# Optimization experiments

Hardware: AMD Instinct MI355X
Metric: run time of the kernel (lower is better)

## Reference

```python
import jax, jax.numpy as jnp
import numpy as np

B, S, H = 16, 64, 4096
NH, NKV, HD = 32, 8, 128
G = NH // NKV
L_CACHE = 4608
ROPE_THETA = 1e6


def setup_inputs() -> dict:
    key = jax.random.key(0)
    ks = jax.random.split(key, 12)
    hidden_states = jax.random.normal(ks[0], (B, S, H), jnp.float32)
    k_cache = jax.random.normal(ks[1], (B, L_CACHE, NKV, HD), jnp.float32)
    v_cache = jax.random.normal(ks[2], (B, L_CACHE, NKV, HD), jnp.float32)
    wq = jax.random.normal(ks[3], (H, H), jnp.float32) * 0.02
    bq = jax.random.normal(ks[4], (H,), jnp.float32) * 0.02
    wk = jax.random.normal(ks[5], (NKV * HD, H), jnp.float32) * 0.02
    bk = jax.random.normal(ks[6], (NKV * HD,), jnp.float32) * 0.02
    wv = jax.random.normal(ks[7], (NKV * HD, H), jnp.float32) * 0.02
    bv = jax.random.normal(ks[8], (NKV * HD,), jnp.float32) * 0.02
    wo = jax.random.normal(ks[9], (H, H), jnp.float32) * 0.02
    cache_lens = jax.random.randint(ks[10], (B,), 2048, 4096, jnp.int32)
    # RoPE cos/sin at absolute positions cache_lens + [0..S)
    inv_freq = 1.0 / (ROPE_THETA ** (jnp.arange(0, HD, 2, dtype=jnp.float32) / HD))
    pos = (cache_lens[:, None] + jnp.arange(S)[None, :]).astype(jnp.float32)  # (B,S)
    freqs = pos[..., None] * inv_freq  # (B,S,HD/2)
    emb = jnp.concatenate([freqs, freqs], axis=-1)  # (B,S,HD)
    cos, sin = jnp.cos(emb), jnp.sin(emb)
    # tree mask: lower-triangular (chain) tree, diagonal included so every query attends
    tree_mask = jnp.tril(jnp.ones((S, S), jnp.bool_))[None].repeat(B, axis=0)
    return {"hidden_states": hidden_states, "cos": cos, "sin": sin,
            "k_cache": k_cache, "v_cache": v_cache,
            "wq": wq, "bq": bq, "wk": wk, "bk": bk, "wv": wv, "bv": bv, "wo": wo,
            "cache_lens": cache_lens, "tree_mask": tree_mask}


def reference(hidden_states, cos, sin, k_cache, v_cache, wq, bq, wk, bk, wv, bv, wo,
              cache_lens, tree_mask):
    scale = 1.0 / jnp.sqrt(jnp.float32(HD))

    def rope(x):  # x: (B,S,h,HD); cos/sin broadcast on head dim (unsqueeze_dim=2)
        x1, x2 = jnp.split(x, 2, axis=-1)
        rot = jnp.concatenate([-x2, x1], axis=-1)
        return x * cos[:, :, None, :] + rot * sin[:, :, None, :]

    q = (hidden_states @ wq.T + bq).reshape(B, S, NH, HD)
    k = (hidden_states @ wk.T + bk).reshape(B, S, NKV, HD)
    v = (hidden_states @ wv.T + bv).reshape(B, S, NKV, HD)
    q, k = rope(q), rope(k)

    # group q heads per kv head: head h = n*G + g (matches repeat_interleave ordering)
    qg = q.reshape(B, S, NKV, G, HD)

    # --- prefix attention against KV cache (flash_attn_with_kvcache semantics) ---
    L = k_cache.shape[1]
    ps = jnp.einsum('bsngd,blnd->bngsl', qg, k_cache) * scale  # (B,NKV,G,S,L)
    valid = jnp.arange(L)[None, :] < cache_lens[:, None]  # (B,L)
    ps = jnp.where(valid[:, None, None, None, :], ps, -jnp.inf)
    prefix_lse = jax.nn.logsumexp(ps, axis=-1)  # (B,NKV,G,S)
    prefix_o = jnp.einsum('bngsl,blnd->bsngd', jax.nn.softmax(ps, axis=-1), v_cache)

    # --- append current k/v into cache and gather (current_kv_len == all_kv_len == S) ---
    pos = cache_lens[:, None] + jnp.arange(S)[None, :]  # (B,S)
    bidx = jnp.arange(B)[:, None]
    k_cache = k_cache.at[bidx, pos].set(k)
    v_cache = v_cache.at[bidx, pos].set(v)
    kc = k_cache[bidx, pos]  # (B,S,NKV,HD)
    vc = v_cache[bidx, pos]

    # --- tree-masked attention over the speculative block ---
    cs = jnp.einsum('bsngd,btnd->bngst', qg, kc) * scale  # (B,NKV,G,S,S)
    cs = jnp.where(tree_mask[:, None, None, :, :], cs, -jnp.inf)
    cur_lse = jax.nn.logsumexp(cs, axis=-1)  # (B,NKV,G,S)
    cur_o = jnp.einsum('bngst,btnd->bsngd', jax.nn.softmax(cs, axis=-1), vc)

    # --- LSE merge of prefix and tree branches ---
    plse = prefix_lse.transpose(0, 3, 1, 2).reshape(B, S, NH)[..., None]
    clse = cur_lse.transpose(0, 3, 1, 2).reshape(B, S, NH)[..., None]
    w = jax.nn.sigmoid(plse - clse)  # (B,S,NH,1)
    out = prefix_o.reshape(B, S, NH, HD) * w + cur_o.reshape(B, S, NH, HD) * (1.0 - w)
    return out.reshape(B, S, H) @ wo.T
```

## Files before the change

### kernel.cpp

```cpp
#include <hip/hip_runtime.h>
#include <stdint.h>
#include <stddef.h>

#define Bb 16
#define Ss 64
#define Hh 4096
#define NKVv 8
#define HDd 128
#define LCACHE 4608
#define MM (Bb*Ss)
#define NQKV (Hh + 2*NKVv*HDd)
#define SCALE_Q 0.08838834764831845f
#define SPLITS 8

typedef float fx4 __attribute__((ext_vector_type(4)));
typedef short s16x8 __attribute__((ext_vector_type(8)));
typedef unsigned short u16;
typedef unsigned short u16x8 __attribute__((ext_vector_type(8)));
typedef unsigned short u16x4 __attribute__((ext_vector_type(4)));

__device__ __forceinline__ u16 f2bf(float f) {
  union { float f; unsigned u; } x; x.f = f;
  unsigned r = x.u + 0x7FFFu + ((x.u >> 16) & 1u);
  return (u16)(r >> 16);
}

__device__ __forceinline__ float bf2f(u16 v) {
  union { unsigned u; float f; } x; x.u = ((unsigned)v) << 16; return x.f;
}

__device__ __forceinline__ fx4 MFMA(s16x8 a, s16x8 b, fx4 c) {
  return __builtin_amdgcn_mfma_f32_16x16x32_bf16(a, b, c, 0, 0, 0);
}

__device__ __forceinline__ void gl_lds16(const void* g, void* l) {
  __builtin_amdgcn_global_load_lds(
      (const __attribute__((address_space(1))) void*)g,
      (__attribute__((address_space(3))) void*)l, 16, 0, 0);
}

__global__ __launch_bounds__(256) void cast_bf16_kernel(
    const float* __restrict__ src, u16* __restrict__ dst, int n8) {
  int i = blockIdx.x * 256 + threadIdx.x;
  if (i >= n8) return;
  fx4 a = *(const fx4*)(src + (size_t)i * 8);
  fx4 b = *(const fx4*)(src + (size_t)i * 8 + 4);
  u16x8 o;
  o[0]=f2bf(a[0]); o[1]=f2bf(a[1]); o[2]=f2bf(a[2]); o[3]=f2bf(a[3]);
  o[4]=f2bf(b[0]); o[5]=f2bf(b[1]); o[6]=f2bf(b[2]); o[7]=f2bf(b[3]);
  *(u16x8*)(dst + (size_t)i * 8) = o;
}

__global__ __launch_bounds__(256) void addf_kernel(
    const float* __restrict__ a, const float* __restrict__ b,
    float* __restrict__ out, int n8) {
  int i = blockIdx.x * 256 + threadIdx.x;
  if (i >= n8) return;
  fx4 x0 = *(const fx4*)(a + (size_t)i * 8);
  fx4 x1 = *(const fx4*)(a + (size_t)i * 8 + 4);
  fx4 y0 = *(const fx4*)(b + (size_t)i * 8);
  fx4 y1 = *(const fx4*)(b + (size_t)i * 8 + 4);
  *(fx4*)(out + (size_t)i * 8)     = x0 + y0;
  *(fx4*)(out + (size_t)i * 8 + 4) = x1 + y1;
}

__global__ __launch_bounds__(256) void gemm_bt_kernel(
    const u16* __restrict__ A, const u16* __restrict__ W,
    const float* __restrict__ bias, float* __restrict__ C,
    int M, int N, int K)
{
  __shared__ __align__(16) u16 As[128*32];
  __shared__ __align__(16) u16 Ws[128*32];
  const int t = threadIdx.x;
  const int lane = t & 63, w = t >> 6;
  const int wr = (w >> 1) * 64, wc = (w & 1) * 64;
  const int lr = lane & 15, lg = lane >> 4;
  const int mt = blockIdx.y * 128, nt = blockIdx.x * 128;
  const int kz = K >> 1;
  const int kbeg = blockIdx.z * kz, kend = kbeg + kz;
  C += (size_t)blockIdx.z * M * N;

  fx4 acc[4][4];
#pragma unroll
  for (int i = 0; i < 4; i++)
#pragma unroll
    for (int j = 0; j < 4; j++) acc[i][j] = (fx4){0.f,0.f,0.f,0.f};

  const int r = t >> 2;
  const int cg = (t & 3) ^ (r & 3);
  const u16* Ag0 = A + (size_t)(mt + r) * K + cg*8;
  const u16* Ag1 = A + (size_t)(mt + 64 + r) * K + cg*8;
  const u16* Wg0 = W + (size_t)(nt + r) * K + cg*8;
  const u16* Wg1 = W + (size_t)(nt + 64 + r) * K + cg*8;
  const int wvb = (t >> 6) * 1024;

  for (int k0 = kbeg; k0 < kend; k0 += 32) {
    __syncthreads();
    gl_lds16(Ag0 + k0, (char*)As + wvb);
    gl_lds16(Ag1 + k0, (char*)As + 4096 + wvb);
    gl_lds16(Wg0 + k0, (char*)Ws + wvb);
    gl_lds16(Wg1 + k0, (char*)Ws + 4096 + wvb);
    __syncthreads();
    s16x8 af[4], bfr[4];
    const int csw = (lg ^ (lr & 3)) * 8;
#pragma unroll
    for (int i = 0; i < 4; i++)
      af[i] = *(const s16x8*)(As + (wr + i*16 + lr)*32 + csw);
#pragma unroll
    for (int j = 0; j < 4; j++)
      bfr[j] = *(const s16x8*)(Ws + (wc + j*16 + lr)*32 + csw);
#pragma unroll
    for (int i = 0; i < 4; i++)
#pragma unroll
      for (int j = 0; j < 4; j++)
        acc[i][j] = MFMA(af[i], bfr[j], acc[i][j]);
  }

#pragma unroll
  for (int j = 0; j < 4; j++) {
    const int col = nt + wc + j*16 + lr;
    const float bv = (bias && blockIdx.z == 0) ? bias[col] : 0.0f;
#pragma unroll
    for (int i = 0; i < 4; i++) {
      const int row0 = mt + wr + i*16 + lg*4;
#pragma unroll
      for (int q = 0; q < 4; q++)
        C[(size_t)(row0 + q) * N + col] = acc[i][j][q] + bv;
    }
  }
}

__global__ __launch_bounds__(256) void rope_split_kernel(
    const float* __restrict__ qkv, const float* __restrict__ cosb,
    const float* __restrict__ sinb, u16* __restrict__ qb,
    u16* __restrict__ kb, u16* __restrict__ vb)
{
  const int wt = blockIdx.x * 4 + (threadIdx.x >> 6);
  const int lane = threadIdx.x & 63;
  const int m = wt / 48;
  const int task = wt - m * 48;
  const int b = m >> 6, s = m & 63;
  const float* row0 = qkv + (size_t)m * NQKV;
  const float* row1 = row0 + (size_t)MM * NQKV;

  if (task < 32) {
    const int h = task;
    const float x1 = row0[h*128 + lane]      + row1[h*128 + lane];
    const float x2 = row0[h*128 + 64 + lane] + row1[h*128 + 64 + lane];
    const float c = cosb[m*128 + lane];
    const float sn = sinb[m*128 + lane];
    u16* dst = qb + (((size_t)(b*8 + (h>>2)))*256 + (h&3)*64 + s) * 128;
    dst[lane]      = f2bf((x1*c - x2*sn) * SCALE_Q);
    dst[lane + 64] = f2bf((x2*c + x1*sn) * SCALE_Q);
  } else if (task < 40) {
    const int n = task - 32;
    const float x1 = row0[4096 + n*128 + lane]      + row1[4096 + n*128 + lane];
    const float x2 = row0[4096 + n*128 + 64 + lane] + row1[4096 + n*128 + 64 + lane];
    const float c = cosb[m*128 + lane];
    const float sn = sinb[m*128 + lane];
    u16* dst = kb + (((size_t)(b*8 + n))*64 + s) * 128;
    dst[lane]      = f2bf(x1*c - x2*sn);
    dst[lane + 64] = f2bf(x2*c + x1*sn);
  } else {
    const int n = task - 40;
    const float x1 = row0[5120 + n*128 + lane]      + row1[5120 + n*128 + lane];
    const float x2 = row0[5120 + n*128 + 64 + lane] + row1[5120 + n*128 + 64 + lane];
    u16* dst = vb + (((size_t)(b*8 + n))*64 + s) * 128;
    dst[lane]      = f2bf(x1);
    dst[lane + 64] = f2bf(x2);
  }
}

__global__ __launch_bounds__(512) void flash_kernel(
    const u16* __restrict__ qb, const u16* __restrict__ kb, const u16* __restrict__ vb,
    const float* __restrict__ kc, const float* __restrict__ vc,
    const int* __restrict__ cache_lens,
    u16* __restrict__ Op, float* __restrict__ lv)
{
  __shared__ __align__(16) u16 Kt[64*128];
  __shared__ __align__(16) u16 Vt[128*64];
  __shared__ __align__(16) u16 Pl[8*32*64];

  const int wid = blockIdx.x;
  const int split = wid & (SPLITS-1);
  const int bn = wid >> 3;
  const int b = bn >> 3, n = bn & 7;
  const int t = threadIdx.x;
  const int lane = t & 63, w = t >> 6;
  const int lr = lane & 15, lg = lane >> 4;
  const int L = cache_lens[b];

  s16x8 qf[2][4];
  const u16* qbase = qb + ((size_t)bn*256 + w*32) * 128;
#pragma unroll
  for (int rf = 0; rf < 2; rf++)
#pragma unroll
    for (int ks = 0; ks < 4; ks++)
      qf[rf][ks] = *(const s16x8*)(qbase + (rf*16 + lr)*128 + ks*32 + lg*8);

  fx4 O[2][8];
  float l_r[2];
#pragma unroll
  for (int rf = 0; rf < 2; rf++) {
    l_r[rf] = 0.f;
#pragma unroll
    for (int cn = 0; cn < 8; cn++) O[rf][cn] = (fx4){0.f,0.f,0.f,0.f};
  }

  const int ntile = (L + 63) >> 6;
  const int chunk = (ntile + SPLITS - 1) / SPLITS;
  const int t0 = split * chunk;
  int t1 = min(t0 + chunk, ntile); if (t1 < t0) t1 = t0;
  const bool last = (split == SPLITS - 1);
  const int tend = last ? t1 + 1 : t1;

  const int krow = t >> 3, kcol = (t & 7) * 16;
  const int vd0 = (t >> 4) * 4, vr0 = (t & 15) * 4;
  char* pw = (char*)Pl + w * 4096;

  const float* kbase = kc + (((size_t)b*LCACHE + krow)*NKVv + n)*HDd + kcol;
  const float* vbase = vc + (((size_t)b*LCACHE + vr0)*NKVv + n)*HDd + vd0;

  fx4 kr0, kr1, kr2, kr3;
#define ISSUEK(tile_) do { \
    const float* ks_ = kbase + (size_t)(tile_) * (64*NKVv*HDd); \
    kr0 = *(const fx4*)(ks_);     kr1 = *(const fx4*)(ks_ + 4); \
    kr2 = *(const fx4*)(ks_ + 8); kr3 = *(const fx4*)(ks_ + 12); \
  } while (0)

  if (t0 < t1) ISSUEK(t0);

  for (int tile = t0; tile < tend; ++tile) {
    const bool cur = (tile == t1);
    const int l0 = tile * 64;
    __syncthreads();
    if (!cur) {
      const float* srcv = vbase + (size_t)tile * (64*NKVv*HDd);
      fx4 vv0 = *(const fx4*)(srcv);
      fx4 vv1 = *(const fx4*)(srcv + NKVv*HDd);
      fx4 vv2 = *(const fx4*)(srcv + 2*NKVv*HDd);
      fx4 vv3 = *(const fx4*)(srcv + 3*NKVv*HDd);
      {
        u16x8 v8;
        v8[0]=f2bf(kr0[0]); v8[1]=f2bf(kr0[1]); v8[2]=f2bf(kr0[2]); v8[3]=f2bf(kr0[3]);
        v8[4]=f2bf(kr1[0]); v8[5]=f2bf(kr1[1]); v8[6]=f2bf(kr1[2]); v8[7]=f2bf(kr1[3]);
        int byt = (krow*256 + kcol*2) ^ ((krow & 7) << 4);
        *(u16x8*)((char*)Kt + byt) = v8;
        v8[0]=f2bf(kr2[0]); v8[1]=f2bf(kr2[1]); v8[2]=f2bf(kr2[2]); v8[3]=f2bf(kr2[3]);
        v8[4]=f2bf(kr3[0]); v8[5]=f2bf(kr3[1]); v8[6]=f2bf(kr3[2]); v8[7]=f2bf(kr3[3]);
        byt = (krow*256 + (kcol + 8)*2) ^ ((krow & 7) << 4);
        *(u16x8*)((char*)Kt + byt) = v8;
      }
      if (tile + 1 < t1) ISSUEK(tile + 1);
      {
#pragma unroll
        for (int dd = 0; dd < 4; dd++) {
          u16x4 pk;
          pk[0]=f2bf(vv0[dd]); pk[1]=f2bf(vv1[dd]); pk[2]=f2bf(vv2[dd]); pk[3]=f2bf(vv3[dd]);
          const int d = vd0 + dd;
          const int byt = (d*128 + vr0*2) ^ ((d & 7) << 4);
          *(u16x4*)((char*)Vt + byt) = pk;
        }
      }
    } else {
      {
        const u16* src = kb + ((size_t)bn*64 + krow)*128 + kcol;
        u16x8 a0 = *(const u16x8*)(src);
        u16x8 a1 = *(const u16x8*)(src + 8);
        int byt = (krow*256 + kcol*2) ^ ((krow & 7) << 4);
        *(u16x8*)((char*)Kt + byt) = a0;
        byt = (krow*256 + (kcol + 8)*2) ^ ((krow & 7) << 4);
        *(u16x8*)((char*)Kt + byt) = a1;
      }
      {
        const u16* srcv = vb + (size_t)bn*8192 + (size_t)vr0*128 + vd0;
        u16x4 tv0 = *(const u16x4*)(srcv);
        u16x4 tv1 = *(const u16x4*)(srcv + 128);
        u16x4 tv2 = *(const u16x4*)(srcv + 256);
        u16x4 tv3 = *(const u16x4*)(srcv + 384);
#pragma unroll
        for (int dd = 0; dd < 4; dd++) {
          u16x4 pk; pk[0]=tv0[dd]; pk[1]=tv1[dd]; pk[2]=tv2[dd]; pk[3]=tv3[dd];
          const int d = vd0 + dd;
          const int byt = (d*128 + vr0*2) ^ ((d & 7) << 4);
          *(u16x4*)((char*)Vt + byt) = pk;
        }
      }
    }
    __syncthreads();

#pragma unroll
    for (int cf = 0; cf < 4; cf++) {
      s16x8 kf[4];
      const int trow = cf*16 + lr;
#pragma unroll
      for (int ks = 0; ks < 4; ks++) {
        const int byt = (trow*256 + (ks*32 + lg*8)*2) ^ ((trow & 7) << 4);
        kf[ks] = *(const s16x8*)((char*)Kt + byt);
      }
#pragma unroll
      for (int rf = 0; rf < 2; rf++) {
        fx4 s = {0.f,0.f,0.f,0.f};
#pragma unroll
        for (int ks = 0; ks < 4; ks++) s = MFMA(kf[ks], qf[rf][ks], s);
        if (cur) {
          const int s0 = ((w*32 + rf*16) & 48) + lr;
#pragma unroll
          for (int i = 0; i < 4; i++)
            if (cf*16 + lg*4 + i > s0) s[i] = -1e30f;
        } else if (l0 + 64 > L) {
          const int kvp = l0 + cf*16 + lg*4;
#pragma unroll
          for (int i = 0; i < 4; i++)
            if (kvp + i >= L) s[i] = -1e30f;
        }
        u16x4 pk;
#pragma unroll
        for (int i = 0; i < 4; i++) {
          const float e = __expf(s[i]);
          l_r[rf] += e;
          pk[i] = f2bf(e);
        }
        const int row = rf*16 + lr;
        const int byt = (row*128 + (cf*16 + lg*4)*2) ^ ((row & 7) << 4);
        *(u16x4*)(pw + byt) = pk;
      }
    }

#pragma unroll
    for (int ksv = 0; ksv < 2; ksv++) {
#pragma unroll
      for (int rf = 0; rf < 2; rf++) {
        const int row = rf*16 + lr;
        const int byt = (row*128 + (ksv*32 + lg*8)*2) ^ ((row & 7) << 4);
        const s16x8 pf = *(const s16x8*)(pw + byt);
#pragma unroll
        for (int cn = 0; cn < 8; cn++) {
          const int c = cn*16 + lr;
          const int bytv = (c*128 + (ksv*32 + lg*8)*2) ^ ((c & 7) << 4);
          const s16x8 vf = *(const s16x8*)((char*)Vt + bytv);
          O[rf][cn] = MFMA(pf, vf, O[rf][cn]);
        }
      }
    }
  }

  const size_t pbase = ((size_t)bn*SPLITS + split) * 256;
#pragma unroll
  for (int rf = 0; rf < 2; rf++) {
    float lt = l_r[rf];
    lt += __shfl_xor(lt, 16);
    lt += __shfl_xor(lt, 32);
    if (lg == 0) lv[pbase + w*32 + rf*16 + lr] = lt;
#pragma unroll
    for (int i = 0; i < 4; i++) {
      const int prow = w*32 + rf*16 + lg*4 + i;
      u16* dst = Op + (pbase + prow)*128;
#pragma unroll
      for (int cn = 0; cn < 8; cn++)
        dst[cn*16 + lr] = f2bf(O[rf][cn][i]);
    }
  }
}

__global__ __launch_bounds__(256) void merge_kernel(
    const u16* __restrict__ Op, const float* __restrict__ lv,
    u16* __restrict__ attn)
{
  const int gid = blockIdx.x * 4 + (threadIdx.x >> 6);
  const int lane = threadIdx.x & 63;
  const int bn = gid >> 8, prow = gid & 255;
  const int b = bn >> 3, n = bn & 7;
  const int g = prow >> 6, srow = prow & 63;

  float ltot = 0.f;
#pragma unroll
  for (int s = 0; s < SPLITS; s++)
    ltot += lv[((size_t)bn*SPLITS + s)*256 + prow];
  const float inv = 1.f / ltot;

  float ox = 0.f, oy = 0.f;
#pragma unroll
  for (int s = 0; s < SPLITS; s++) {
    const u16* src = Op + (((size_t)bn*SPLITS + s)*256 + prow)*128 + lane*2;
    ox += bf2f(src[0]);
    oy += bf2f(src[1]);
  }
  u16* dst = attn + ((size_t)(b*64 + srow))*4096 + (size_t)(n*4 + g)*128 + lane*2;
  dst[0] = f2bf(ox * inv);
  dst[1] = f2bf(oy * inv);
}

extern "C" void kernel_launch(void* const* d_in, const int* in_sizes, int n_in,
                              void* d_out, int out_size, void* d_ws, size_t ws_size,
                              hipStream_t stream) {
  (void)in_sizes; (void)n_in; (void)out_size; (void)ws_size;
  const float* hidden = (const float*)d_in[0];
  const float* cosb   = (const float*)d_in[1];
  const float* sinb   = (const float*)d_in[2];
  const float* kc     = (const float*)d_in[3];
  const float* vc     = (const float*)d_in[4];
  const float* wq     = (const float*)d_in[5];
  const float* bq     = (const float*)d_in[6];
  const float* wk     = (const float*)d_in[7];
  const float* bk     = (const float*)d_in[8];
  const float* wv     = (const float*)d_in[9];
  const float* bv     = (const float*)d_in[10];
  const float* wo     = (const float*)d_in[11];
  const int* clens    = (const int*)d_in[12];
  float* out = (float*)d_out;

  char* ws = (char*)d_ws;
  size_t off = 0;
  auto alloc = [&](size_t bytes) -> void* {
    void* p = ws + off; off += (bytes + 255) & ~(size_t)255; return p;
  };
  u16* Wqkv  = (u16*)alloc((size_t)NQKV * Hh * 2);
  u16* Xb    = (u16*)alloc((size_t)MM * Hh * 2);
  float* qkvf= (float*)alloc((size_t)2 * MM * NQKV * 4);
  u16* qbuf  = (u16*)alloc((size_t)Bb*NKVv*256*HDd*2);
  u16* kbuf  = (u16*)alloc((size_t)Bb*NKVv*64*HDd*2);
  u16* vbuf  = (u16*)alloc((size_t)Bb*NKVv*64*HDd*2);
  float* biasq = (float*)alloc((size_t)NQKV * 4);
  u16* Op    = (u16*)alloc((size_t)Bb*NKVv*SPLITS*256*128*2);
  float* lv  = (float*)alloc((size_t)Bb*NKVv*SPLITS*256*4);

  hipMemcpyAsync(biasq,        bq, 4096*sizeof(float), hipMemcpyDeviceToDevice, stream);
  hipMemcpyAsync(biasq + 4096, bk, 1024*sizeof(float), hipMemcpyDeviceToDevice, stream);
  hipMemcpyAsync(biasq + 5120, bv, 1024*sizeof(float), hipMemcpyDeviceToDevice, stream);

  auto cast = [&](const float* s, u16* d, size_t nelem) {
    int n8 = (int)(nelem / 8);
    cast_bf16_kernel<<<(n8 + 255) / 256, 256, 0, stream>>>(s, d, n8);
  };
  cast(hidden, Xb, (size_t)MM * Hh);
  cast(wq, Wqkv,                      (size_t)4096 * 4096);
  cast(wk, Wqkv + (size_t)4096*4096,  (size_t)1024 * 4096);
  cast(wv, Wqkv + (size_t)5120*4096,  (size_t)1024 * 4096);

  gemm_bt_kernel<<<dim3(NQKV/128, MM/128, 2), 256, 0, stream>>>(Xb, Wqkv, biasq, qkvf, MM, NQKV, Hh);
  rope_split_kernel<<<(MM*48)/4, 256, 0, stream>>>(qkvf, cosb, sinb, qbuf, kbuf, vbuf);

  u16* Wo = Wqkv;
  cast(wo, Wo, (size_t)4096 * 4096);

  flash_kernel<<<Bb*NKVv*SPLITS, 512, 0, stream>>>(qbuf, kbuf, vbuf, kc, vc, clens, Op, lv);

  u16* attn = Xb;
  merge_kernel<<<(Bb*NKVv*256)/4, 256, 0, stream>>>(Op, lv, attn);

  float* Cp = qkvf;
  gemm_bt_kernel<<<dim3(Hh/128, MM/128, 2), 256, 0, stream>>>(attn, Wo, nullptr, Cp, MM, Hh, Hh);
  addf_kernel<<<((MM*Hh/8) + 255)/256, 256, 0, stream>>>(Cp, Cp + (size_t)MM*Hh, out, MM*Hh/8);
}
```

Measured before the change: 377.8 us.

## Drop split-K GEMMs, use 128x64 tiles with XCD remap, fuse casts, add MFMA priority

Replaces the split-K=2 GEMMs, which wrote two fp32 partials that were then summed, with single-pass GEMMs on 128x64 tiles and an XCD-aware block remap. This removes the extra partial-sum traffic, the addf kernel and the doubled reads in rope. All five fp32-to-bf16 casts are merged into one launch, with Wo getting its own buffer. The flash kernel wraps its MFMA sections in s_setprio and reuses each V fragment for both row tiles. Each GEMM now runs fewer, longer blocks (768 and 512), which may reduce latency hiding compared with split-K.

```diff
diff --git a/kernel.cpp b/kernel.cpp
--- a/kernel.cpp
+++ b/kernel.cpp
@@ -39,29 +39,26 @@
       (__attribute__((address_space(3))) void*)l, 16, 0, 0);
 }
 
-__global__ __launch_bounds__(256) void cast_bf16_kernel(
-    const float* __restrict__ src, u16* __restrict__ dst, int n8) {
-  int i = blockIdx.x * 256 + threadIdx.x;
-  if (i >= n8) return;
-  fx4 a = *(const fx4*)(src + (size_t)i * 8);
-  fx4 b = *(const fx4*)(src + (size_t)i * 8 + 4);
+__global__ __launch_bounds__(256) void cast_all_kernel(
+    const float* __restrict__ hid, const float* __restrict__ wq,
+    const float* __restrict__ wk, const float* __restrict__ wv,
+    const float* __restrict__ wo, u16* __restrict__ xb,
+    u16* __restrict__ wqkv, u16* __restrict__ wob)
+{
+  const int bid = blockIdx.x;
+  const float* src; u16* dst; long i;
+  if (bid < 2048)       { src = hid; dst = xb;   i = (long)bid * 256; }
+  else if (bid < 10240) { src = wq;  dst = wqkv; i = (long)(bid - 2048) * 256; }
+  else if (bid < 12288) { src = wk;  dst = wqkv + (size_t)4096*4096; i = (long)(bid - 10240) * 256; }
+  else if (bid < 14336) { src = wv;  dst = wqkv + (size_t)5120*4096; i = (long)(bid - 12288) * 256; }
+  else                  { src = wo;  dst = wob;  i = (long)(bid - 14336) * 256; }
+  i += threadIdx.x;
+  fx4 a = *(const fx4*)(src + i * 8);
+  fx4 b = *(const fx4*)(src + i * 8 + 4);
   u16x8 o;
   o[0]=f2bf(a[0]); o[1]=f2bf(a[1]); o[2]=f2bf(a[2]); o[3]=f2bf(a[3]);
   o[4]=f2bf(b[0]); o[5]=f2bf(b[1]); o[6]=f2bf(b[2]); o[7]=f2bf(b[3]);
-  *(u16x8*)(dst + (size_t)i * 8) = o;
-}
-
-__global__ __launch_bounds__(256) void addf_kernel(
-    const float* __restrict__ a, const float* __restrict__ b,
-    float* __restrict__ out, int n8) {
-  int i = blockIdx.x * 256 + threadIdx.x;
-  if (i >= n8) return;
-  fx4 x0 = *(const fx4*)(a + (size_t)i * 8);
-  fx4 x1 = *(const fx4*)(a + (size_t)i * 8 + 4);
-  fx4 y0 = *(const fx4*)(b + (size_t)i * 8);
-  fx4 y1 = *(const fx4*)(b + (size_t)i * 8 + 4);
-  *(fx4*)(out + (size_t)i * 8)     = x0 + y0;
-  *(fx4*)(out + (size_t)i * 8 + 4) = x1 + y1;
+  *(u16x8*)(dst + i * 8) = o;
 }
 
 __global__ __launch_bounds__(256) void gemm_bt_kernel(
@@ -70,56 +67,59 @@
     int M, int N, int K)
 {
   __shared__ __align__(16) u16 As[128*32];
-  __shared__ __align__(16) u16 Ws[128*32];
+  __shared__ __align__(16) u16 Ws[64*32];
   const int t = threadIdx.x;
   const int lane = t & 63, w = t >> 6;
-  const int wr = (w >> 1) * 64, wc = (w & 1) * 64;
+  const int wr = (w >> 1) * 64, wc = (w & 1) * 32;
   const int lr = lane & 15, lg = lane >> 4;
-  const int mt = blockIdx.y * 128, nt = blockIdx.x * 128;
-  const int kz = K >> 1;
-  const int kbeg = blockIdx.z * kz, kend = kbeg + kz;
-  C += (size_t)blockIdx.z * M * N;
-
-  fx4 acc[4][4];
+
+  const int nwg = gridDim.x;
+  const int cpx = nwg >> 3;
+  const int wid = (blockIdx.x & 7) * cpx + (blockIdx.x >> 3);
+  const int Nt = N >> 6;
+  const int nt = (wid % Nt) * 64;
+  const int mt = (wid / Nt) * 128;
+
+  fx4 acc[4][2];
 #pragma unroll
   for (int i = 0; i < 4; i++)
 #pragma unroll
-    for (int j = 0; j < 4; j++) acc[i][j] = (fx4){0.f,0.f,0.f,0.f};
+    for (int j = 0; j < 2; j++) acc[i][j] = (fx4){0.f,0.f,0.f,0.f};
 
   const int r = t >> 2;
   const int cg = (t & 3) ^ (r & 3);
   const u16* Ag0 = A + (size_t)(mt + r) * K + cg*8;
   const u16* Ag1 = A + (size_t)(mt + 64 + r) * K + cg*8;
   const u16* Wg0 = W + (size_t)(nt + r) * K + cg*8;
-  const u16* Wg1 = W + (size_t)(nt + 64 + r) * K + cg*8;
-  const int wvb = (t >> 6) * 1024;
-
-  for (int k0 = kbeg; k0 < kend; k0 += 32) {
+  const int wvb = w * 1024;
+
+  for (int k0 = 0; k0 < K; k0 += 32) {
     __syncthreads();
     gl_lds16(Ag0 + k0, (char*)As + wvb);
     gl_lds16(Ag1 + k0, (char*)As + 4096 + wvb);
     gl_lds16(Wg0 + k0, (char*)Ws + wvb);
-    gl_lds16(Wg1 + k0, (char*)Ws + 4096 + wvb);
     __syncthreads();
-    s16x8 af[4], bfr[4];
+    s16x8 af[4], bfr[2];
     const int csw = (lg ^ (lr & 3)) * 8;
 #pragma unroll
     for (int i = 0; i < 4; i++)
       af[i] = *(const s16x8*)(As + (wr + i*16 + lr)*32 + csw);
 #pragma unroll
-    for (int j = 0; j < 4; j++)
+    for (int j = 0; j < 2; j++)
       bfr[j] = *(const s16x8*)(Ws + (wc + j*16 + lr)*32 + csw);
+    __builtin_amdgcn_s_setprio(1);
 #pragma unroll
     for (int i = 0; i < 4; i++)
 #pragma unroll
-      for (int j = 0; j < 4; j++)
+      for (int j = 0; j < 2; j++)
         acc[i][j] = MFMA(af[i], bfr[j], acc[i][j]);
-  }
-
-#pragma unroll
-  for (int j = 0; j < 4; j++) {
+    __builtin_amdgcn_s_setprio(0);
+  }
+
+#pragma unroll
+  for (int j = 0; j < 2; j++) {
     const int col = nt + wc + j*16 + lr;
-    const float bv = (bias && blockIdx.z == 0) ? bias[col] : 0.0f;
+    const float bv = bias ? bias[col] : 0.0f;
 #pragma unroll
     for (int i = 0; i < 4; i++) {
       const int row0 = mt + wr + i*16 + lg*4;
@@ -140,13 +140,12 @@
   const int m = wt / 48;
   const int task = wt - m * 48;
   const int b = m >> 6, s = m & 63;
-  const float* row0 = qkv + (size_t)m * NQKV;
-  const float* row1 = row0 + (size_t)MM * NQKV;
+  const float* row = qkv + (size_t)m * NQKV;
 
   if (task < 32) {
     const int h = task;
-    const float x1 = row0[h*128 + lane]      + row1[h*128 + lane];
-    const float x2 = row0[h*128 + 64 + lane] + row1[h*128 + 64 + lane];
+    const float x1 = row[h*128 + lane];
+    const float x2 = row[h*128 + 64 + lane];
     const float c = cosb[m*128 + lane];
     const float sn = sinb[m*128 + lane];
     u16* dst = qb + (((size_t)(b*8 + (h>>2)))*256 + (h&3)*64 + s) * 128;
@@ -154,8 +153,8 @@
     dst[lane + 64] = f2bf((x2*c + x1*sn) * SCALE_Q);
   } else if (task < 40) {
     const int n = task - 32;
-    const float x1 = row0[4096 + n*128 + lane]      + row1[4096 + n*128 + lane];
-    const float x2 = row0[4096 + n*128 + 64 + lane] + row1[4096 + n*128 + 64 + lane];
+    const float x1 = row[4096 + n*128 + lane];
+    const float x2 = row[4096 + n*128 + 64 + lane];
     const float c = cosb[m*128 + lane];
     const float sn = sinb[m*128 + lane];
     u16* dst = kb + (((size_t)(b*8 + n))*64 + s) * 128;
@@ -163,8 +162,8 @@
     dst[lane + 64] = f2bf(x2*c + x1*sn);
   } else {
     const int n = task - 40;
-    const float x1 = row0[5120 + n*128 + lane]      + row1[5120 + n*128 + lane];
-    const float x2 = row0[5120 + n*128 + 64 + lane] + row1[5120 + n*128 + 64 + lane];
+    const float x1 = row[5120 + n*128 + lane];
+    const float x2 = row[5120 + n*128 + 64 + lane];
     u16* dst = vb + (((size_t)(b*8 + n))*64 + s) * 128;
     dst[lane]      = f2bf(x1);
     dst[lane + 64] = f2bf(x2);
@@ -298,11 +297,19 @@
         const int byt = (trow*256 + (ks*32 + lg*8)*2) ^ ((trow & 7) << 4);
         kf[ks] = *(const s16x8*)((char*)Kt + byt);
       }
+      fx4 sc2[2];
+      __builtin_amdgcn_s_setprio(1);
 #pragma unroll
       for (int rf = 0; rf < 2; rf++) {
         fx4 s = {0.f,0.f,0.f,0.f};
 #pragma unroll
         for (int ks = 0; ks < 4; ks++) s = MFMA(kf[ks], qf[rf][ks], s);
+        sc2[rf] = s;
+      }
+      __builtin_amdgcn_s_setprio(0);
+#pragma unroll
+      for (int rf = 0; rf < 2; rf++) {
+        fx4 s = sc2[rf];
         if (cur) {
           const int s0 = ((w*32 + rf*16) & 48) + lr;
 #pragma unroll
@@ -329,19 +336,20 @@
 
 #pragma unroll
     for (int ksv = 0; ksv < 2; ksv++) {
-#pragma unroll
-      for (int rf = 0; rf < 2; rf++) {
-        const int row = rf*16 + lr;
-        const int byt = (row*128 + (ksv*32 + lg*8)*2) ^ ((row & 7) << 4);
-        const s16x8 pf = *(const s16x8*)(pw + byt);
-#pragma unroll
-        for (int cn = 0; cn < 8; cn++) {
-          const int c = cn*16 + lr;
-          const int bytv = (c*128 + (ksv*32 + lg*8)*2) ^ ((c & 7) << 4);
-          const s16x8 vf = *(const s16x8*)((char*)Vt + bytv);
-          O[rf][cn] = MFMA(pf, vf, O[rf][cn]);
-        }
-      }
+      const int bytp0 = (lr*128 + (ksv*32 + lg*8)*2) ^ ((lr & 7) << 4);
+      const s16x8 pf0 = *(const s16x8*)(pw + bytp0);
+      const int bytp1 = ((16 + lr)*128 + (ksv*32 + lg*8)*2) ^ ((lr & 7) << 4);
+      const s16x8 pf1 = *(const s16x8*)(pw + bytp1);
+      __builtin_amdgcn_s_setprio(1);
+#pragma unroll
+      for (int cn = 0; cn < 8; cn++) {
+        const int c = cn*16 + lr;
+        const int bytv = (c*128 + (ksv*32 + lg*8)*2) ^ ((c & 7) << 4);
+        const s16x8 vf = *(const s16x8*)((char*)Vt + bytv);
+        O[0][cn] = MFMA(pf0, vf, O[0][cn]);
+        O[1][cn] = MFMA(pf1, vf, O[1][cn]);
+      }
+      __builtin_amdgcn_s_setprio(0);
     }
   }
 
@@ -416,8 +424,9 @@
     void* p = ws + off; off += (bytes + 255) & ~(size_t)255; return p;
   };
   u16* Wqkv  = (u16*)alloc((size_t)NQKV * Hh * 2);
+  u16* Wob   = (u16*)alloc((size_t)Hh * Hh * 2);
   u16* Xb    = (u16*)alloc((size_t)MM * Hh * 2);
-  float* qkvf= (float*)alloc((size_t)2 * MM * NQKV * 4);
+  float* qkvf= (float*)alloc((size_t)MM * NQKV * 4);
   u16* qbuf  = (u16*)alloc((size_t)Bb*NKVv*256*HDd*2);
   u16* kbuf  = (u16*)alloc((size_t)Bb*NKVv*64*HDd*2);
   u16* vbuf  = (u16*)alloc((size_t)Bb*NKVv*64*HDd*2);
@@ -429,27 +438,15 @@
   hipMemcpyAsync(biasq + 4096, bk, 1024*sizeof(float), hipMemcpyDeviceToDevice, stream);
   hipMemcpyAsync(biasq + 5120, bv, 1024*sizeof(float), hipMemcpyDeviceToDevice, stream);
 
-  auto cast = [&](const float* s, u16* d, size_t nelem) {
-    int n8 = (int)(nelem / 8);
-    cast_bf16_kernel<<<(n8 + 255) / 256, 256, 0, stream>>>(s, d, n8);
-  };
-  cast(hidden, Xb, (size_t)MM * Hh);
-  cast(wq, Wqkv,                      (size_t)4096 * 4096);
-  cast(wk, Wqkv + (size_t)4096*4096,  (size_t)1024 * 4096);
-  cast(wv, Wqkv + (size_t)5120*4096,  (size_t)1024 * 4096);
-
-  gemm_bt_kernel<<<dim3(NQKV/128, MM/128, 2), 256, 0, stream>>>(Xb, Wqkv, biasq, qkvf, MM, NQKV, Hh);
+  cast_all_kernel<<<22528, 256, 0, stream>>>(hidden, wq, wk, wv, wo, Xb, Wqkv, Wob);
+
+  gemm_bt_kernel<<<768, 256, 0, stream>>>(Xb, Wqkv, biasq, qkvf, MM, NQKV, Hh);
   rope_split_kernel<<<(MM*48)/4, 256, 0, stream>>>(qkvf, cosb, sinb, qbuf, kbuf, vbuf);
-
-  u16* Wo = Wqkv;
-  cast(wo, Wo, (size_t)4096 * 4096);
 
   flash_kernel<<<Bb*NKVv*SPLITS, 512, 0, stream>>>(qbuf, kbuf, vbuf, kc, vc, clens, Op, lv);
 
   u16* attn = Xb;
   merge_kernel<<<(Bb*NKVv*256)/4, 256, 0, stream>>>(Op, lv, attn);
 
-  float* Cp = qkvf;
-  gemm_bt_kernel<<<dim3(Hh/128, MM/128, 2), 256, 0, stream>>>(attn, Wo, nullptr, Cp, MM, Hh, Hh);
-  addf_kernel<<<((MM*Hh/8) + 255)/256, 256, 0, stream>>>(Cp, Cp + (size_t)MM*Hh, out, MM*Hh/8);
-}
+  gemm_bt_kernel<<<512, 256, 0, stream>>>(attn, Wob, nullptr, out, MM, Hh, Hh);
+}
```

Result: slower. 403.3 us (+6.7%).

## Fuse input casts, drop bias memcpys, add MFMA setprio and share V fragments

Applied to the files above, without the earlier changes.

Replaces the four separate fp32-to-bf16 cast launches with one combined cast kernel. It also removes the three device-to-device bias copies by having the GEMM epilogue pick bq, bk or bv by column. The GEMM and flash kernels wrap their MFMA bursts in s_setprio to favour matrix issue. The PV loop now loads each V fragment once and reuses it for both row fragments, which cuts LDS reads. Together these reduce launch and copy overhead, at the cost of a per-column branch in the epilogue.

```diff
diff --git a/kernel.cpp b/kernel.cpp
--- a/kernel.cpp
+++ b/kernel.cpp
@@ -37,6 +37,26 @@
   __builtin_amdgcn_global_load_lds(
       (const __attribute__((address_space(1))) void*)g,
       (__attribute__((address_space(3))) void*)l, 16, 0, 0);
+}
+
+__global__ __launch_bounds__(256) void cast_all_kernel(
+    const float* __restrict__ hid, const float* __restrict__ wq,
+    const float* __restrict__ wk, const float* __restrict__ wv,
+    u16* __restrict__ xb, u16* __restrict__ wqkv)
+{
+  const int bid = blockIdx.x;
+  const float* src; u16* dst; long i;
+  if (bid < 2048)       { src = hid; dst = xb;   i = (long)bid * 256; }
+  else if (bid < 10240) { src = wq;  dst = wqkv; i = (long)(bid - 2048) * 256; }
+  else if (bid < 12288) { src = wk;  dst = wqkv + (size_t)4096*4096; i = (long)(bid - 10240) * 256; }
+  else                  { src = wv;  dst = wqkv + (size_t)5120*4096; i = (long)(bid - 12288) * 256; }
+  i += threadIdx.x;
+  fx4 a = *(const fx4*)(src + i * 8);
+  fx4 b = *(const fx4*)(src + i * 8 + 4);
+  u16x8 o;
+  o[0]=f2bf(a[0]); o[1]=f2bf(a[1]); o[2]=f2bf(a[2]); o[3]=f2bf(a[3]);
+  o[4]=f2bf(b[0]); o[5]=f2bf(b[1]); o[6]=f2bf(b[2]); o[7]=f2bf(b[3]);
+  *(u16x8*)(dst + i * 8) = o;
 }
 
 __global__ __launch_bounds__(256) void cast_bf16_kernel(
@@ -66,7 +86,8 @@
 
 __global__ __launch_bounds__(256) void gemm_bt_kernel(
     const u16* __restrict__ A, const u16* __restrict__ W,
-    const float* __restrict__ bias, float* __restrict__ C,
+    const float* __restrict__ bqp, const float* __restrict__ bkp,
+    const float* __restrict__ bvp, float* __restrict__ C,
     int M, int N, int K)
 {
   __shared__ __align__(16) u16 As[128*32];
@@ -92,7 +113,7 @@
   const u16* Ag1 = A + (size_t)(mt + 64 + r) * K + cg*8;
   const u16* Wg0 = W + (size_t)(nt + r) * K + cg*8;
   const u16* Wg1 = W + (size_t)(nt + 64 + r) * K + cg*8;
-  const int wvb = (t >> 6) * 1024;
+  const int wvb = w * 1024;
 
   for (int k0 = kbeg; k0 < kend; k0 += 32) {
     __syncthreads();
@@ -109,23 +130,27 @@
 #pragma unroll
     for (int j = 0; j < 4; j++)
       bfr[j] = *(const s16x8*)(Ws + (wc + j*16 + lr)*32 + csw);
+    __builtin_amdgcn_s_setprio(1);
 #pragma unroll
     for (int i = 0; i < 4; i++)
 #pragma unroll
       for (int j = 0; j < 4; j++)
         acc[i][j] = MFMA(af[i], bfr[j], acc[i][j]);
+    __builtin_amdgcn_s_setprio(0);
   }
 
 #pragma unroll
   for (int j = 0; j < 4; j++) {
     const int col = nt + wc + j*16 + lr;
-    const float bv = (bias && blockIdx.z == 0) ? bias[col] : 0.0f;
+    float bv_ = 0.0f;
+    if (bqp && blockIdx.z == 0)
+      bv_ = col < 4096 ? bqp[col] : (col < 5120 ? bkp[col - 4096] : bvp[col - 5120]);
 #pragma unroll
     for (int i = 0; i < 4; i++) {
       const int row0 = mt + wr + i*16 + lg*4;
 #pragma unroll
       for (int q = 0; q < 4; q++)
-        C[(size_t)(row0 + q) * N + col] = acc[i][j][q] + bv;
+        C[(size_t)(row0 + q) * N + col] = acc[i][j][q] + bv_;
     }
   }
 }
@@ -298,11 +323,19 @@
         const int byt = (trow*256 + (ks*32 + lg*8)*2) ^ ((trow & 7) << 4);
         kf[ks] = *(const s16x8*)((char*)Kt + byt);
       }
+      fx4 sc2[2];
+      __builtin_amdgcn_s_setprio(1);
 #pragma unroll
       for (int rf = 0; rf < 2; rf++) {
         fx4 s = {0.f,0.f,0.f,0.f};
 #pragma unroll
         for (int ks = 0; ks < 4; ks++) s = MFMA(kf[ks], qf[rf][ks], s);
+        sc2[rf] = s;
+      }
+      __builtin_amdgcn_s_setprio(0);
+#pragma unroll
+      for (int rf = 0; rf < 2; rf++) {
+        fx4 s = sc2[rf];
         if (cur) {
           const int s0 = ((w*32 + rf*16) & 48) + lr;
 #pragma unroll
@@ -329,19 +362,20 @@
 
 #pragma unroll
     for (int ksv = 0; ksv < 2; ksv++) {
-#pragma unroll
-      for (int rf = 0; rf < 2; rf++) {
-        const int row = rf*16 + lr;
-        const int byt = (row*128 + (ksv*32 + lg*8)*2) ^ ((row & 7) << 4);
-        const s16x8 pf = *(const s16x8*)(pw + byt);
-#pragma unroll
-        for (int cn = 0; cn < 8; cn++) {
-          const int c = cn*16 + lr;
-          const int bytv = (c*128 + (ksv*32 + lg*8)*2) ^ ((c & 7) << 4);
-          const s16x8 vf = *(const s16x8*)((char*)Vt + bytv);
-          O[rf][cn] = MFMA(pf, vf, O[rf][cn]);
-        }
-      }
+      const int bytp0 = (lr*128 + (ksv*32 + lg*8)*2) ^ ((lr & 7) << 4);
+      const s16x8 pf0 = *(const s16x8*)(pw + bytp0);
+      const int bytp1 = ((16 + lr)*128 + (ksv*32 + lg*8)*2) ^ ((lr & 7) << 4);
+      const s16x8 pf1 = *(const s16x8*)(pw + bytp1);
+      __builtin_amdgcn_s_setprio(1);
+#pragma unroll
+      for (int cn = 0; cn < 8; cn++) {
+        const int c = cn*16 + lr;
+        const int bytv = (c*128 + (ksv*32 + lg*8)*2) ^ ((c & 7) << 4);
+        const s16x8 vf = *(const s16x8*)((char*)Vt + bytv);
+        O[0][cn] = MFMA(pf0, vf, O[0][cn]);
+        O[1][cn] = MFMA(pf1, vf, O[1][cn]);
+      }
+      __builtin_amdgcn_s_setprio(0);
     }
   }
 
@@ -421,28 +455,17 @@
   u16* qbuf  = (u16*)alloc((size_t)Bb*NKVv*256*HDd*2);
   u16* kbuf  = (u16*)alloc((size_t)Bb*NKVv*64*HDd*2);
   u16* vbuf  = (u16*)alloc((size_t)Bb*NKVv*64*HDd*2);
-  float* biasq = (float*)alloc((size_t)NQKV * 4);
   u16* Op    = (u16*)alloc((size_t)Bb*NKVv*SPLITS*256*128*2);
   float* lv  = (float*)alloc((size_t)Bb*NKVv*SPLITS*256*4);
 
-  hipMemcpyAsync(biasq,        bq, 4096*sizeof(float), hipMemcpyDeviceToDevice, stream);
-  hipMemcpyAsync(biasq + 4096, bk, 1024*sizeof(float), hipMemcpyDeviceToDevice, stream);
-  hipMemcpyAsync(biasq + 5120, bv, 1024*sizeof(float), hipMemcpyDeviceToDevice, stream);
-
-  auto cast = [&](const float* s, u16* d, size_t nelem) {
-    int n8 = (int)(nelem / 8);
-    cast_bf16_kernel<<<(n8 + 255) / 256, 256, 0, stream>>>(s, d, n8);
-  };
-  cast(hidden, Xb, (size_t)MM * Hh);
-  cast(wq, Wqkv,                      (size_t)4096 * 4096);
-  cast(wk, Wqkv + (size_t)4096*4096,  (size_t)1024 * 4096);
-  cast(wv, Wqkv + (size_t)5120*4096,  (size_t)1024 * 4096);
-
-  gemm_bt_kernel<<<dim3(NQKV/128, MM/128, 2), 256, 0, stream>>>(Xb, Wqkv, biasq, qkvf, MM, NQKV, Hh);
+  cast_all_kernel<<<14336, 256, 0, stream>>>(hidden, wq, wk, wv, Xb, Wqkv);
+
+  gemm_bt_kernel<<<dim3(NQKV/128, MM/128, 2), 256, 0, stream>>>(
+      Xb, Wqkv, bq, bk, bv, qkvf, MM, NQKV, Hh);
   rope_split_kernel<<<(MM*48)/4, 256, 0, stream>>>(qkvf, cosb, sinb, qbuf, kbuf, vbuf);
 
   u16* Wo = Wqkv;
-  cast(wo, Wo, (size_t)4096 * 4096);
+  cast_bf16_kernel<<<8192, 256, 0, stream>>>(wo, Wo, (int)(((size_t)Hh*Hh)/8));
 
   flash_kernel<<<Bb*NKVv*SPLITS, 512, 0, stream>>>(qbuf, kbuf, vbuf, kc, vc, clens, Op, lv);
 
@@ -450,6 +473,7 @@
   merge_kernel<<<(Bb*NKVv*256)/4, 256, 0, stream>>>(Op, lv, attn);
 
   float* Cp = qkvf;
-  gemm_bt_kernel<<<dim3(Hh/128, MM/128, 2), 256, 0, stream>>>(attn, Wo, nullptr, Cp, MM, Hh, Hh);
+  gemm_bt_kernel<<<dim3(Hh/128, MM/128, 2), 256, 0, stream>>>(
+      attn, Wo, nullptr, nullptr, nullptr, Cp, MM, Hh, Hh);
   addf_kernel<<<((MM*Hh/8) + 255)/256, 256, 0, stream>>>(Cp, Cp + (size_t)MM*Hh, out, MM*Hh/8);
 }
```

Result: faster. 360.6 us (-4.6%).
